# Optimization experiments

Measured on AMD Instinct MI355X. Metric: run time of the kernel, lower is better.

The kernel has to match this reference:

```python
import jax, jax.numpy as jnp
import numpy as np
import math

EMBED_DIM = 2048
NUM_HEADS = 32
GROUPS = 4
HEAD_DIM = EMBED_DIM // NUM_HEADS  # 64
HPG = NUM_HEADS // GROUPS          # heads per group = 8


def setup_inputs() -> dict:
    key = jax.random.key(0)
    k_x, k_wq, k_bq, k_wkv, k_bkv = jax.random.split(key, 5)
    B, L = 4, 4096
    scale = 1.0 / math.sqrt(EMBED_DIM)
    return {
        "x": jax.random.normal(k_x, (B, L, EMBED_DIM), dtype=jnp.float32),
        "Wq": jax.random.normal(k_wq, (EMBED_DIM, EMBED_DIM), dtype=jnp.float32) * scale,
        "bq": jax.random.normal(k_bq, (EMBED_DIM,), dtype=jnp.float32) * 0.01,
        "Wkv": jax.random.normal(k_wkv, (EMBED_DIM, 2 * HEAD_DIM * GROUPS), dtype=jnp.float32) * scale,
        "bkv": jax.random.normal(k_bkv, (2 * HEAD_DIM * GROUPS,), dtype=jnp.float32) * 0.01,
    }


def reference(x, Wq, bq, Wkv, bkv):
    B, L, _ = x.shape
    # projections
    q = (x @ Wq + bq).reshape(B, L, GROUPS, HPG, HEAD_DIM)          # blghd
    kv = (x @ Wkv + bkv).reshape(B, L, GROUPS, 2, HEAD_DIM)
    k, v = kv[:, :, :, 0], kv[:, :, :, 1]                            # blgd
    # scores: q @ k^T with k of shape (..., 1, head_dim) -> (..., HPG, 1)
    scores = jnp.einsum("blghd,blgd->blgh", q, k)[..., None] / math.sqrt(HEAD_DIM)
    attn = jax.nn.softmax(scores, axis=-1)                           # size-1 axis -> ones
    # attn @ v: (..., HPG, 1) @ (..., 1, head_dim) -> (..., HPG, head_dim)
    out = attn * v[:, :, :, None, :]                                 # blghd
    return out.reshape(B, L, EMBED_DIM)
```

## Files before the change

### kernel.cpp

```cpp
#include <hip/hip_runtime.h>


#define EMBED 2048
#define BK 64
#define KIT (EMBED / BK)
#define SA 72
#define SV 68

typedef _Float16 half8 __attribute__((ext_vector_type(8)));
typedef _Float16 half4v __attribute__((ext_vector_type(4)));
typedef float f32x4 __attribute__((ext_vector_type(4)));

#define BAR() asm volatile("s_waitcnt lgkmcnt(0)\ns_barrier" ::: "memory")

__global__ __launch_bounds__(256) void prep_b(const float* __restrict__ Wkv,
                                              _Float16* __restrict__ Bt) {
  const int t = threadIdx.x;
  const int kb = blockIdx.x * 4;
  const int vcol = ((t >> 6) * 128) + 64 + (t & 63);
  float v[4];
#pragma unroll
  for (int i = 0; i < 4; ++i) v[i] = Wkv[(size_t)(kb + i) * 512 + vcol];
  half4v h;
#pragma unroll
  for (int i = 0; i < 4; ++i) h[i] = (_Float16)v[i];
  *(half4v*)&Bt[(size_t)t * EMBED + kb] = h;
}

__global__ __launch_bounds__(256, 4) void gqa_main(
    const float* __restrict__ x, const _Float16* __restrict__ Bt,
    const float* __restrict__ bkv, float* __restrict__ out) {
  __shared__ __align__(16) char smem[2 * 64 * SA * 2];
  _Float16* As = (_Float16*)smem;
  _Float16* Bs = As + 64 * SA;
  float* Vs = (float*)smem;

  const int tid = threadIdx.x;
  const int wave = tid >> 6;
  const int lane = tid & 63;
  const int lm = lane & 15;
  const int lq = lane >> 4;
  const int bi = blockIdx.x;
  const int nb = (bi >> 3) & 3;
  const int mb = ((bi >> 5) << 3) | (bi & 7);
  const int mi2 = wave & 1;
  const int ni2 = wave >> 1;

  const int ar = tid >> 4, ac = (tid & 15) * 4;
  const float* ap = x + (size_t)(mb * 64 + ar) * EMBED + ac;
  _Float16* aw = As + ar * SA + ac;
  const int br = tid >> 2, bc = (tid & 3) * 8;
  const _Float16* bp = Bt + (size_t)(nb * 64 + br) * EMBED + bc;
  _Float16* bw = Bs + br * SA + bc;

  const _Float16* ard = As + (mi2 * 32 + lm) * SA + lq * 8;
  const _Float16* brd = Bs + (ni2 * 32 + lm) * SA + lq * 8;

  f32x4 pa0[4], pa1[4];
  half8 pb0[2], pb1[2];

#define LOADAB(kt, PA, PB)                       \
  {                                              \
    const float* p_ = ap + (kt) * BK;            \
    PA[0] = *(const f32x4*)p_;                   \
    PA[1] = *(const f32x4*)(p_ + 16 * EMBED);    \
    PA[2] = *(const f32x4*)(p_ + 32 * EMBED);    \
    PA[3] = *(const f32x4*)(p_ + 48 * EMBED);    \
    const _Float16* q_ = bp + (kt) * BK;         \
    PB[0] = *(const half8*)q_;                   \
    PB[1] = *(const half8*)(q_ + 32);            \
  }
#define STAGE(PA, PB)                            \
  {                                              \
    _Pragma("unroll") for (int c_ = 0; c_ < 4; ++c_) { \
      half4v h_;                                 \
      _Pragma("unroll") for (int j_ = 0; j_ < 4; ++j_) \
          h_[j_] = (_Float16)PA[c_][j_];         \
      *(half4v*)(aw + c_ * 16 * SA) = h_;        \
    }                                            \
    *(half8*)bw = PB[0];                         \
    *(half8*)(bw + 32) = PB[1];                  \
  }
#define COMPUTE()                                                         \
  {                                                                       \
    half8 af_[2][2], bf_[2][2];                                           \
    _Pragma("unroll") for (int mi_ = 0; mi_ < 2; ++mi_)                   \
        _Pragma("unroll") for (int ks_ = 0; ks_ < 2; ++ks_)               \
            af_[mi_][ks_] = *(const half8*)(ard + mi_ * 16 * SA + ks_ * 32); \
    _Pragma("unroll") for (int ni_ = 0; ni_ < 2; ++ni_)                   \
        _Pragma("unroll") for (int ks_ = 0; ks_ < 2; ++ks_)               \
            bf_[ni_][ks_] = *(const half8*)(brd + ni_ * 16 * SA + ks_ * 32); \
    _Pragma("unroll") for (int mi_ = 0; mi_ < 2; ++mi_)                   \
        _Pragma("unroll") for (int ni_ = 0; ni_ < 2; ++ni_)               \
            _Pragma("unroll") for (int ks_ = 0; ks_ < 2; ++ks_)           \
                acc[mi_][ni_] = __builtin_amdgcn_mfma_f32_16x16x32_f16(   \
                    af_[mi_][ks_], bf_[ni_][ks_], acc[mi_][ni_], 0, 0, 0); \
  }

  f32x4 acc[2][2] = {};

  LOADAB(0, pa0, pb0);
  LOADAB(1, pa1, pb1);

  for (int kt = 0; kt < KIT; kt += 2) {
    STAGE(pa0, pb0);
    BAR();
    if (kt + 2 < KIT) LOADAB(kt + 2, pa0, pb0);
    COMPUTE();
    BAR();
    STAGE(pa1, pb1);
    BAR();
    if (kt + 3 < KIT) LOADAB(kt + 3, pa1, pb1);
    COMPUTE();
    BAR();
  }

#pragma unroll
  for (int ni = 0; ni < 2; ++ni) {
    const int nc = ni2 * 32 + ni * 16 + lm;
    const float bias = bkv[nb * 128 + 64 + nc];
#pragma unroll
    for (int mi = 0; mi < 2; ++mi) {
      f32x4 v = acc[mi][ni];
#pragma unroll
      for (int r = 0; r < 4; ++r) {
        Vs[(mi2 * 32 + mi * 16 + lq * 4 + r) * SV + nc] = v[r] + bias;
      }
    }
  }
  BAR();

  f32x4* out4 = (f32x4*)(out + (size_t)(mb * 64) * EMBED + nb * 512);
#pragma unroll 8
  for (int i = 0; i < 32; ++i) {
    const int f = i * 256 + tid;
    const int row = f >> 7;
    const int c4 = f & 127;
    const int d4 = c4 & 15;
    out4[(size_t)row * 512 + c4] = *(const f32x4*)&Vs[row * SV + d4 * 4];
  }
}

extern "C" void kernel_launch(void* const* d_in, const int* in_sizes, int n_in,
                              void* d_out, int out_size, void* d_ws, size_t ws_size,
                              hipStream_t stream) {
  const float* x = (const float*)d_in[0];
  const float* Wkv = (const float*)d_in[3];
  const float* bkv = (const float*)d_in[4];
  float* out = (float*)d_out;
  _Float16* Bt = (_Float16*)d_ws;

  prep_b<<<512, 256, 0, stream>>>(Wkv, Bt);
  gqa_main<<<1024, 256, 0, stream>>>(x, Bt, bkv, out);
}
```

Before: 279.1 us.

## Halve M tile to 32 rows, double grid and occupancy

Shrinks each block's output tile from 64x64 to 32x64 rows of x, doubling the grid to 2048 blocks and raising the launch-bounds occupancy hint to 8 blocks per CU. Each wave now computes a single 16-row M fragment against two N fragments, and global loads are reshaped into wider contiguous per-thread chunks. The goal is more parallelism and latency hiding for this memory-bound projection. The cost is that each block re-reads the B tile for half as many rows and issues fewer MFMAs per LDS load.

New measurement: 308.9 us. 1.11x slower.

```diff
diff --git a/kernel.cpp b/kernel.cpp
--- a/kernel.cpp
+++ b/kernel.cpp
@@ -27,12 +27,12 @@
   *(half4v*)&Bt[(size_t)t * EMBED + kb] = h;
 }
 
-__global__ __launch_bounds__(256, 4) void gqa_main(
+__global__ __launch_bounds__(256, 8) void gqa_main(
     const float* __restrict__ x, const _Float16* __restrict__ Bt,
     const float* __restrict__ bkv, float* __restrict__ out) {
-  __shared__ __align__(16) char smem[2 * 64 * SA * 2];
+  __shared__ __align__(16) char smem[(32 + 64) * SA * 2];
   _Float16* As = (_Float16*)smem;
-  _Float16* Bs = As + 64 * SA;
+  _Float16* Bs = As + 32 * SA;
   float* Vs = (float*)smem;
 
   const int tid = threadIdx.x;
@@ -46,58 +46,54 @@
   const int mi2 = wave & 1;
   const int ni2 = wave >> 1;
 
-  const int ar = tid >> 4, ac = (tid & 15) * 4;
-  const float* ap = x + (size_t)(mb * 64 + ar) * EMBED + ac;
+  const int ar = tid >> 3, ac = (tid & 7) * 8;
+  const float* ap = x + (size_t)(mb * 32 + ar) * EMBED + ac;
   _Float16* aw = As + ar * SA + ac;
-  const int br = tid >> 2, bc = (tid & 3) * 8;
+  const int br = tid >> 2, bc = (tid & 3) * 16;
   const _Float16* bp = Bt + (size_t)(nb * 64 + br) * EMBED + bc;
   _Float16* bw = Bs + br * SA + bc;
 
-  const _Float16* ard = As + (mi2 * 32 + lm) * SA + lq * 8;
+  const _Float16* ard = As + (mi2 * 16 + lm) * SA + lq * 8;
   const _Float16* brd = Bs + (ni2 * 32 + lm) * SA + lq * 8;
 
-  f32x4 pa0[4], pa1[4];
+  f32x4 pa0[2], pa1[2];
   half8 pb0[2], pb1[2];
 
 #define LOADAB(kt, PA, PB)                       \
   {                                              \
     const float* p_ = ap + (kt) * BK;            \
     PA[0] = *(const f32x4*)p_;                   \
-    PA[1] = *(const f32x4*)(p_ + 16 * EMBED);    \
-    PA[2] = *(const f32x4*)(p_ + 32 * EMBED);    \
-    PA[3] = *(const f32x4*)(p_ + 48 * EMBED);    \
+    PA[1] = *(const f32x4*)(p_ + 4);             \
     const _Float16* q_ = bp + (kt) * BK;         \
     PB[0] = *(const half8*)q_;                   \
-    PB[1] = *(const half8*)(q_ + 32);            \
+    PB[1] = *(const half8*)(q_ + 8);             \
   }
 #define STAGE(PA, PB)                            \
   {                                              \
-    _Pragma("unroll") for (int c_ = 0; c_ < 4; ++c_) { \
-      half4v h_;                                 \
-      _Pragma("unroll") for (int j_ = 0; j_ < 4; ++j_) \
-          h_[j_] = (_Float16)PA[c_][j_];         \
-      *(half4v*)(aw + c_ * 16 * SA) = h_;        \
-    }                                            \
+    half8 h_;                                    \
+    _Pragma("unroll") for (int j_ = 0; j_ < 4; ++j_) \
+        h_[j_] = (_Float16)PA[0][j_];            \
+    _Pragma("unroll") for (int j_ = 0; j_ < 4; ++j_) \
+        h_[4 + j_] = (_Float16)PA[1][j_];        \
+    *(half8*)aw = h_;                            \
     *(half8*)bw = PB[0];                         \
-    *(half8*)(bw + 32) = PB[1];                  \
+    *(half8*)(bw + 8) = PB[1];                   \
   }
 #define COMPUTE()                                                         \
   {                                                                       \
-    half8 af_[2][2], bf_[2][2];                                           \
-    _Pragma("unroll") for (int mi_ = 0; mi_ < 2; ++mi_)                   \
-        _Pragma("unroll") for (int ks_ = 0; ks_ < 2; ++ks_)               \
-            af_[mi_][ks_] = *(const half8*)(ard + mi_ * 16 * SA + ks_ * 32); \
+    half8 af_[2], bf_[2][2];                                              \
+    _Pragma("unroll") for (int ks_ = 0; ks_ < 2; ++ks_)                   \
+        af_[ks_] = *(const half8*)(ard + ks_ * 32);                       \
     _Pragma("unroll") for (int ni_ = 0; ni_ < 2; ++ni_)                   \
         _Pragma("unroll") for (int ks_ = 0; ks_ < 2; ++ks_)               \
             bf_[ni_][ks_] = *(const half8*)(brd + ni_ * 16 * SA + ks_ * 32); \
-    _Pragma("unroll") for (int mi_ = 0; mi_ < 2; ++mi_)                   \
-        _Pragma("unroll") for (int ni_ = 0; ni_ < 2; ++ni_)               \
-            _Pragma("unroll") for (int ks_ = 0; ks_ < 2; ++ks_)           \
-                acc[mi_][ni_] = __builtin_amdgcn_mfma_f32_16x16x32_f16(   \
-                    af_[mi_][ks_], bf_[ni_][ks_], acc[mi_][ni_], 0, 0, 0); \
+    _Pragma("unroll") for (int ni_ = 0; ni_ < 2; ++ni_)                   \
+        _Pragma("unroll") for (int ks_ = 0; ks_ < 2; ++ks_)               \
+            acc[ni_] = __builtin_amdgcn_mfma_f32_16x16x32_f16(            \
+                af_[ks_], bf_[ni_][ks_], acc[ni_], 0, 0, 0);              \
   }
 
-  f32x4 acc[2][2] = {};
+  f32x4 acc[2] = {};
 
   LOADAB(0, pa0, pb0);
   LOADAB(1, pa1, pb1);
@@ -119,20 +115,17 @@
   for (int ni = 0; ni < 2; ++ni) {
     const int nc = ni2 * 32 + ni * 16 + lm;
     const float bias = bkv[nb * 128 + 64 + nc];
+    f32x4 v = acc[ni];
 #pragma unroll
-    for (int mi = 0; mi < 2; ++mi) {
-      f32x4 v = acc[mi][ni];
-#pragma unroll
-      for (int r = 0; r < 4; ++r) {
-        Vs[(mi2 * 32 + mi * 16 + lq * 4 + r) * SV + nc] = v[r] + bias;
-      }
+    for (int r = 0; r < 4; ++r) {
+      Vs[(mi2 * 16 + lq * 4 + r) * SV + nc] = v[r] + bias;
     }
   }
   BAR();
 
-  f32x4* out4 = (f32x4*)(out + (size_t)(mb * 64) * EMBED + nb * 512);
+  f32x4* out4 = (f32x4*)(out + (size_t)(mb * 32) * EMBED + nb * 512);
 #pragma unroll 8
-  for (int i = 0; i < 32; ++i) {
+  for (int i = 0; i < 16; ++i) {
     const int f = i * 256 + tid;
     const int row = f >> 7;
     const int c4 = f & 127;
@@ -151,5 +144,5 @@
   _Float16* Bt = (_Float16*)d_ws;
 
   prep_b<<<512, 256, 0, stream>>>(Wkv, Bt);
-  gqa_main<<<1024, 256, 0, stream>>>(x, Bt, bkv, out);
+  gqa_main<<<2048, 256, 0, stream>>>(x, Bt, bkv, out);
 }
```
